# Optimization experiments

Measured on AMD Instinct MI355X. Metric: run time of the kernel, lower is better.

Reference implementation:

```python
import jax, jax.numpy as jnp
import numpy as np

N_HEAD = 16
SCALE = True
NEG = 10000.0


def setup_inputs() -> dict:
    key = jax.random.key(0)
    ks = jax.random.split(key, 5)
    B, S, D = 4, 1024, 1024
    x = jax.random.normal(ks[0], (B, S, D), dtype=jnp.float32)
    # GPT-2 Conv1D weights: W has shape [in, out], init ~N(0, 0.02)
    w_attn = jax.random.normal(ks[1], (D, 3 * D), dtype=jnp.float32) * 0.02
    b_attn = jnp.zeros((3 * D,), dtype=jnp.float32)
    w_proj = jax.random.normal(ks[2], (D, D), dtype=jnp.float32) * 0.02
    b_proj = jnp.zeros((D,), dtype=jnp.float32)
    return {"x": x, "w_attn": w_attn, "b_attn": b_attn,
            "w_proj": w_proj, "b_proj": b_proj}


def reference(x, w_attn, b_attn, w_proj, b_proj):
    B, S, D = x.shape
    H = N_HEAD
    hd = D // H
    # c_attn: Conv1D == x @ W + b
    qkv = jnp.einsum('bsd,de->bse', x, w_attn) + b_attn
    q, k, v = jnp.split(qkv, 3, axis=-1)
    # split heads -> [B, H, S, hd]
    q = q.reshape(B, S, H, hd).transpose(0, 2, 1, 3)
    k = k.reshape(B, S, H, hd).transpose(0, 2, 1, 3)
    v = v.reshape(B, S, H, hd).transpose(0, 2, 1, 3)
    # scores [B, H, S, S]
    w = jnp.einsum('bhqd,bhkd->bhqk', q, k)
    if SCALE:
        w = w / jnp.sqrt(jnp.float32(hd))
    # multiplicative causal mask: w*b - 10000*(1-b)
    bmask = jnp.tril(jnp.ones((S, S), dtype=w.dtype))[None, None]
    w = w * bmask - NEG * (1.0 - bmask)
    w = jax.nn.softmax(w, axis=-1)
    # attn_pdrop = 0 -> dropout is identity
    a = jnp.einsum('bhqk,bhkd->bhqd', w, v)
    # merge heads
    a = a.transpose(0, 2, 1, 3).reshape(B, S, D)
    # c_proj; resid_pdrop = 0
    out = jnp.einsum('bsd,de->bse', a, w_proj) + b_proj
    return out
```

## Files before the change

kernel.cpp:

```cpp
#include <hip/hip_runtime.h>
#include <hip/hip_bf16.h>


typedef __bf16 bf16x8 __attribute__((ext_vector_type(8)));
typedef float f32x4 __attribute__((ext_vector_type(4)));

__device__ __forceinline__ void load_lds16(const void* g, void* l) {
  __builtin_amdgcn_global_load_lds(
      (const __attribute__((address_space(1))) void*)g,
      (__attribute__((address_space(3))) void*)l, 16, 0, 0);
}

__global__ __launch_bounds__(256) void prep(
    const float* __restrict__ x, const float* __restrict__ w_attn,
    const float* __restrict__ w_proj, __bf16* __restrict__ Xb,
    __bf16* __restrict__ WT_attn, __bf16* __restrict__ WT_proj) {
  __shared__ __bf16 tile[32][33];
  const int blk = blockIdx.x;
  const int tid = threadIdx.x;
  if (blk < 4096) {
    const float* W;
    __bf16* WT;
    int n0, k0, N;
    if (blk < 3072) {
      W = w_attn; WT = WT_attn; N = 3072;
      n0 = (blk % 96) * 32; k0 = (blk / 96) * 32;
    } else {
      W = w_proj; WT = WT_proj; N = 1024;
      const int t = blk - 3072;
      n0 = (t & 31) * 32; k0 = (t >> 5) * 32;
    }
    const int tx = tid & 31, ty = tid >> 5;
#pragma unroll
    for (int j = 0; j < 32; j += 8)
      tile[ty + j][tx] = (__bf16)W[(size_t)(k0 + ty + j) * N + n0 + tx];
    __syncthreads();
#pragma unroll
    for (int j = 0; j < 32; j += 8)
      WT[(size_t)(n0 + ty + j) * 1024 + k0 + tx] = tile[tx][ty + j];
  } else {
    const size_t i = (size_t)(blk - 4096) * 4096 + tid * 16;
    const float4* xp = (const float4*)(x + i);
    float4 a = xp[0], b = xp[1], c = xp[2], d = xp[3];
    bf16x8 o0, o1;
    o0[0] = (__bf16)a.x; o0[1] = (__bf16)a.y; o0[2] = (__bf16)a.z; o0[3] = (__bf16)a.w;
    o0[4] = (__bf16)b.x; o0[5] = (__bf16)b.y; o0[6] = (__bf16)b.z; o0[7] = (__bf16)b.w;
    o1[0] = (__bf16)c.x; o1[1] = (__bf16)c.y; o1[2] = (__bf16)c.z; o1[3] = (__bf16)c.w;
    o1[4] = (__bf16)d.x; o1[5] = (__bf16)d.y; o1[6] = (__bf16)d.z; o1[7] = (__bf16)d.w;
    *(bf16x8*)(Xb + i) = o0;
    *(bf16x8*)(Xb + i + 8) = o1;
  }
}

__global__ __launch_bounds__(256) void transpose_v(
    const __bf16* __restrict__ Vr, __bf16* __restrict__ VT) {
  const int lane = threadIdx.x & 63, wave = threadIdx.x >> 6;
  const int bh = blockIdx.x >> 4;
  const int kb = (blockIdx.x & 15) * 64;
  const int b = bh >> 4, h = bh & 15;
  const __bf16* src =
      Vr + (size_t)(b * 1024 + kb + lane) * 1024 + h * 64 + wave * 16;
  bf16x8 v0 = *(const bf16x8*)src;
  bf16x8 v1 = *(const bf16x8*)(src + 8);
  __bf16* dst = VT + ((size_t)bh * 64 + wave * 16) * 1024 + kb + lane;
#pragma unroll
  for (int i = 0; i < 8; ++i) {
    dst[(size_t)i * 1024] = v0[i];
    dst[(size_t)(i + 8) * 1024] = v1[i];
  }
}

#define GEMM_CORE(A_, BT_, K_)                                                   \
  __shared__ __bf16 sA[128 * 32];                                               \
  __shared__ __bf16 sB[128 * 32];                                               \
  const int tid = threadIdx.x;                                                  \
  const int lane = tid & 63;                                                    \
  const int wave = tid >> 6;                                                    \
  const int waveM = wave >> 1, waveN = wave & 1;                                \
  const int quad = lane >> 4;                                                   \
  const int l16 = lane & 15;                                                    \
  const int rowBase = blockIdx.y * 128;                                         \
  const int colBase = blockIdx.x * 128;                                         \
  const int rIn = lane >> 2;                                                    \
  const int sIn = lane & 3;                                                     \
  const int gc = sIn ^ (rIn & 3) ^ ((rIn >> 2) & 3);                            \
  const int readSlot = quad ^ (l16 & 3) ^ ((l16 >> 2) & 3);                     \
  f32x4 acc[4][4] = {};                                                         \
  for (int k0 = 0; k0 < K_; k0 += 32) {                                         \
    __syncthreads();                                                            \
    _Pragma("unroll") for (int j = 0; j < 2; ++j) {                             \
      const int rb = wave * 32 + j * 16;                                        \
      load_lds16(&A_[(size_t)(rowBase + rb + rIn) * K_ + k0 + gc * 8],          \
                 &sA[rb * 32]);                                                 \
      load_lds16(&BT_[(size_t)(colBase + rb + rIn) * K_ + k0 + gc * 8],         \
                 &sB[rb * 32]);                                                 \
    }                                                                           \
    __syncthreads();                                                            \
    bf16x8 af[4], bfr[4];                                                       \
    _Pragma("unroll") for (int mt = 0; mt < 4; ++mt)                            \
      af[mt] = *(const bf16x8*)(&sA[(waveM * 64 + mt * 16 + l16) * 32 +         \
                                    readSlot * 8]);                             \
    _Pragma("unroll") for (int nt = 0; nt < 4; ++nt)                            \
      bfr[nt] = *(const bf16x8*)(&sB[(waveN * 64 + nt * 16 + l16) * 32 +        \
                                     readSlot * 8]);                            \
    _Pragma("unroll") for (int mt = 0; mt < 4; ++mt)                            \
    _Pragma("unroll") for (int nt = 0; nt < 4; ++nt)                            \
      acc[mt][nt] = __builtin_amdgcn_mfma_f32_16x16x32_bf16(                    \
          af[mt], bfr[nt], acc[mt][nt], 0, 0, 0);                               \
  }

__global__ __launch_bounds__(256) void gemm_qkv(
    const __bf16* __restrict__ A, const __bf16* __restrict__ BT,
    const float* __restrict__ bias, __bf16* __restrict__ Qp,
    __bf16* __restrict__ Kp, __bf16* __restrict__ Vr) {
  GEMM_CORE(A, BT, 1024)
  const int seg = colBase >> 10;
#pragma unroll
  for (int mt = 0; mt < 4; ++mt) {
    const int row0 = rowBase + waveM * 64 + mt * 16 + quad * 4;
#pragma unroll
    for (int nt = 0; nt < 4; ++nt) {
      const int col = colBase + waveN * 64 + nt * 16 + l16;
      const float bv = bias[col];
      const int cc = col & 1023;
#pragma unroll
      for (int r = 0; r < 4; ++r) {
        const int row = row0 + r;
        const float v = acc[mt][nt][r] + bv;
        if (seg == 2) {
          Vr[(size_t)row * 1024 + cc] = (__bf16)v;
        } else {
          const int bh = ((row >> 10) << 4) + (cc >> 6);
          __bf16* dst = (seg == 0) ? Qp : Kp;
          dst[((size_t)bh << 16) + (size_t)(row & 1023) * 64 + (cc & 63)] =
              (__bf16)v;
        }
      }
    }
  }
}

__global__ __launch_bounds__(256) void gemm_out(
    const __bf16* __restrict__ A, const __bf16* __restrict__ BT,
    const float* __restrict__ bias, float* __restrict__ C) {
  GEMM_CORE(A, BT, 1024)
#pragma unroll
  for (int mt = 0; mt < 4; ++mt) {
    const int row = rowBase + waveM * 64 + mt * 16 + quad * 4;
#pragma unroll
    for (int nt = 0; nt < 4; ++nt) {
      const int col = colBase + waveN * 64 + nt * 16 + l16;
      const float bv = bias[col];
#pragma unroll
      for (int r = 0; r < 4; ++r)
        C[(size_t)(row + r) * 1024 + col] = acc[mt][nt][r] + bv;
    }
  }
}

__global__ __launch_bounds__(256) void attn_mfma(
    const __bf16* __restrict__ Qp, const __bf16* __restrict__ Kp,
    const __bf16* __restrict__ VT, __bf16* __restrict__ Aout) {
  __shared__ __bf16 sK[128 * 64];
  __shared__ __bf16 sV[64 * 128];
  __shared__ __bf16 sP[4 * 16 * 128];

  const int tid = threadIdx.x;
  const int lane = tid & 63;
  const int wave = tid >> 6;
  const int quad = lane >> 4;
  const int l16 = lane & 15;
  const int swq = l16 & 7;

  const int bh = blockIdx.x >> 3;
  const int pr = blockIdx.x & 7;
  const int b = bh >> 4, h = bh & 15;
  const int qbA = pr * 64, qbB = (15 - pr) * 64;
  const int ktA_max = pr >> 1, ktB_max = (15 - pr) >> 1;

  const __bf16* Qb = Qp + ((size_t)bh << 16);
  const __bf16* Kb = Kp + ((size_t)bh << 16);
  const __bf16* VTb = VT + (size_t)bh * 64 * 1024;

  bf16x8 qA0A, qA1A, qA0B, qA1B;
  {
    const __bf16* qr = Qb + (size_t)(qbA + wave * 16 + l16) * 64 + quad * 8;
    qA0A = *(const bf16x8*)qr;
    qA1A = *(const bf16x8*)(qr + 32);
    qr = Qb + (size_t)(qbB + wave * 16 + l16) * 64 + quad * 8;
    qA0B = *(const bf16x8*)qr;
    qA1B = *(const bf16x8*)(qr + 32);
  }

  f32x4 OA[4] = {}, OB[4] = {};
  float psA[4] = {0.f, 0.f, 0.f, 0.f}, psB[4] = {0.f, 0.f, 0.f, 0.f};
  __bf16* pw = sP + wave * 2048;

  for (int kt = 0; kt <= ktB_max; ++kt) {
    const int kb = kt * 128;
    __syncthreads();

#pragma unroll
    for (int i = 0; i < 4; ++i) {
      const int rb = wave * 32 + i * 8;
      load_lds16(Kb + (size_t)(kb + rb + (lane >> 3)) * 64 +
                     (((lane & 7) ^ ((lane >> 3) & 7)) << 3),
                 &sK[rb * 64]);
    }
#pragma unroll
    for (int i = 0; i < 4; ++i) {
      const int db = wave * 16 + i * 4;
      const int d = db + (lane >> 4);
      load_lds16(VTb + (size_t)d * 1024 + kb + (((lane & 15) ^ (d & 7)) << 3),
                 &sV[db * 128]);
    }
    __syncthreads();

    {
      float sc[8][4];
#pragma unroll
      for (int n = 0; n < 8; ++n) {
        const int key = n * 16 + l16;
        bf16x8 kB0 = *(const bf16x8*)(&sK[key * 64 + ((quad ^ swq) << 3)]);
        bf16x8 kB1 = *(const bf16x8*)(&sK[key * 64 + (((quad + 4) ^ swq) << 3)]);
        f32x4 c = {};
        c = __builtin_amdgcn_mfma_f32_16x16x32_bf16(qA0B, kB0, c, 0, 0, 0);
        c = __builtin_amdgcn_mfma_f32_16x16x32_bf16(qA1B, kB1, c, 0, 0, 0);
#pragma unroll
        for (int r = 0; r < 4; ++r) sc[n][r] = c[r] * 0.125f;
      }
      if (kt == ktB_max) {
#pragma unroll
        for (int n = 0; n < 8; ++n) {
          const int kg = kb + n * 16 + l16;
#pragma unroll
          for (int r = 0; r < 4; ++r)
            if (kg > qbB + wave * 16 + quad * 4 + r) sc[n][r] = -1.0e30f;
        }
      }
#pragma unroll
      for (int n = 0; n < 8; ++n)
#pragma unroll
        for (int r = 0; r < 4; ++r) {
          float p = __expf(fminf(sc[n][r], 60.0f));
          sc[n][r] = p;
          psB[r] += p;
        }
      {
        const int kb8 = l16 >> 3, lo = l16 & 7;
#pragma unroll
        for (int n = 0; n < 8; ++n) {
          const int chunk = n * 2 + kb8;
#pragma unroll
          for (int r = 0; r < 4; ++r) {
            const int q = quad * 4 + r;
            pw[q * 128 + ((chunk ^ (q & 7)) << 3) + lo] = (__bf16)sc[n][r];
          }
        }
      }
#pragma unroll
      for (int cc = 0; cc < 4; ++cc) {
        bf16x8 pA = *(const bf16x8*)(&pw[l16 * 128 + (((cc * 4 + quad) ^ swq) << 3)]);
#pragma unroll
        for (int nt = 0; nt < 4; ++nt) {
          bf16x8 vB = *(const bf16x8*)(&sV[(nt * 16 + l16) * 128 +
                                           (((cc * 4 + quad) ^ swq) << 3)]);
          OB[nt] = __builtin_amdgcn_mfma_f32_16x16x32_bf16(pA, vB, OB[nt], 0, 0, 0);
        }
      }
    }

    if (kt <= ktA_max) {
      float sc[8][4];
#pragma unroll
      for (int n = 0; n < 8; ++n) {
        const int key = n * 16 + l16;
        bf16x8 kB0 = *(const bf16x8*)(&sK[key * 64 + ((quad ^ swq) << 3)]);
        bf16x8 kB1 = *(const bf16x8*)(&sK[key * 64 + (((quad + 4) ^ swq) << 3)]);
        f32x4 c = {};
        c = __builtin_amdgcn_mfma_f32_16x16x32_bf16(qA0A, kB0, c, 0, 0, 0);
        c = __builtin_amdgcn_mfma_f32_16x16x32_bf16(qA1A, kB1, c, 0, 0, 0);
#pragma unroll
        for (int r = 0; r < 4; ++r) sc[n][r] = c[r] * 0.125f;
      }
      if (kt == ktA_max) {
#pragma unroll
        for (int n = 0; n < 8; ++n) {
          const int kg = kb + n * 16 + l16;
#pragma unroll
          for (int r = 0; r < 4; ++r)
            if (kg > qbA + wave * 16 + quad * 4 + r) sc[n][r] = -1.0e30f;
        }
      }
#pragma unroll
      for (int n = 0; n < 8; ++n)
#pragma unroll
        for (int r = 0; r < 4; ++r) {
          float p = __expf(fminf(sc[n][r], 60.0f));
          sc[n][r] = p;
          psA[r] += p;
        }
      {
        const int kb8 = l16 >> 3, lo = l16 & 7;
#pragma unroll
        for (int n = 0; n < 8; ++n) {
          const int chunk = n * 2 + kb8;
#pragma unroll
          for (int r = 0; r < 4; ++r) {
            const int q = quad * 4 + r;
            pw[q * 128 + ((chunk ^ (q & 7)) << 3) + lo] = (__bf16)sc[n][r];
          }
        }
      }
#pragma unroll
      for (int cc = 0; cc < 4; ++cc) {
        bf16x8 pA = *(const bf16x8*)(&pw[l16 * 128 + (((cc * 4 + quad) ^ swq) << 3)]);
#pragma unroll
        for (int nt = 0; nt < 4; ++nt) {
          bf16x8 vB = *(const bf16x8*)(&sV[(nt * 16 + l16) * 128 +
                                           (((cc * 4 + quad) ^ swq) << 3)]);
          OA[nt] = __builtin_amdgcn_mfma_f32_16x16x32_bf16(pA, vB, OA[nt], 0, 0, 0);
        }
      }
    }
  }

  float invA[4], invB[4];
#pragma unroll
  for (int r = 0; r < 4; ++r) {
    float pa = psA[r], pb = psB[r];
    pa += __shfl_xor(pa, 1); pb += __shfl_xor(pb, 1);
    pa += __shfl_xor(pa, 2); pb += __shfl_xor(pb, 2);
    pa += __shfl_xor(pa, 4); pb += __shfl_xor(pb, 4);
    pa += __shfl_xor(pa, 8); pb += __shfl_xor(pb, 8);
    invA[r] = 1.0f / pa;
    invB[r] = 1.0f / pb;
  }
#pragma unroll
  for (int nt = 0; nt < 4; ++nt) {
#pragma unroll
    for (int r = 0; r < 4; ++r) {
      const int qA = qbA + wave * 16 + quad * 4 + r;
      const int qB = qbB + wave * 16 + quad * 4 + r;
      Aout[((size_t)b * 1024 + qA) * 1024 + h * 64 + nt * 16 + l16] =
          (__bf16)(OA[nt][r] * invA[r]);
      Aout[((size_t)b * 1024 + qB) * 1024 + h * 64 + nt * 16 + l16] =
          (__bf16)(OB[nt][r] * invB[r]);
    }
  }
}

extern "C" void kernel_launch(void* const* d_in, const int* in_sizes, int n_in,
                              void* d_out, int out_size, void* d_ws,
                              size_t ws_size, hipStream_t stream) {
  const float* x      = (const float*)d_in[0];
  const float* w_attn = (const float*)d_in[1];
  const float* b_attn = (const float*)d_in[2];
  const float* w_proj = (const float*)d_in[3];
  const float* b_proj = (const float*)d_in[4];
  float* out = (float*)d_out;

  char* ws = (char*)d_ws;
  __bf16* WT_attn = (__bf16*)(ws);
  __bf16* WT_proj = (__bf16*)(ws + 6291456);
  __bf16* Xb      = (__bf16*)(ws + 8388608);
  __bf16* Qp      = (__bf16*)(ws + 16777216);
  __bf16* Kp      = (__bf16*)(ws + 25165824);
  __bf16* Vr      = (__bf16*)(ws + 33554432);
  __bf16* Aattn   = (__bf16*)(ws + 41943040);
  __bf16* VT      = Xb;

  prep<<<5120, 256, 0, stream>>>(x, w_attn, w_proj, Xb, WT_attn, WT_proj);
  gemm_qkv<<<dim3(24, 32), 256, 0, stream>>>(Xb, WT_attn, b_attn, Qp, Kp, Vr);
  transpose_v<<<1024, 256, 0, stream>>>(Vr, VT);
  attn_mfma<<<512, 256, 0, stream>>>(Qp, Kp, VT, Aattn);
  gemm_out<<<dim3(8, 32), 256, 0, stream>>>(Aattn, WT_proj, b_proj, out);
}
```

Before: 180.3 us.

## Rewrite QKV GEMM as 256x256-tile 8-wave kernel with ping-pong LDS pipeline

Replaces the 128x128-tile QKV GEMM with a 512-thread kernel computing 256x256 tiles over 192 blocks. It double-buffers 64-wide K slices in 128 KB of LDS using direct global-to-LDS loads, XOR-swizzled LDS reads and a barrier-interleaved schedule that overlaps loads with MFMA quarter-phases. It also raises wave priority around MFMA bursts and remaps block indices for cache locality. The goal is to cut global traffic per FLOP and hide memory latency, at the cost of fewer blocks than CUs (192 tiles) and many barriers.

Result: no change. 178.9 us (-0.8%).

```diff
diff --git a/kernel.cpp b/kernel.cpp
--- a/kernel.cpp
+++ b/kernel.cpp
@@ -109,24 +109,156 @@
           af[mt], bfr[nt], acc[mt][nt], 0, 0, 0);                               \
   }
 
-__global__ __launch_bounds__(256) void gemm_qkv(
+
+#define BAR8 asm volatile("s_barrier" ::: "memory")
+#define LGKM0 asm volatile("s_waitcnt lgkmcnt(0)" ::: "memory")
+
+#define STG(GMAT, GROW0, K0, LOFF)                                             \
+  _Pragma("unroll") for (int i_ = 0; i_ < 2; ++i_)                             \
+    load_lds16((GMAT) + (size_t)((GROW0) + i_ * 64 + wave * 8 + srow) * 1024 + \
+                   (K0) + schunk * 8,                                          \
+               smem8 + (LOFF) + (i_ * 64 + wave * 8) * 64);
+
+#define LDA8(BASE, MH)                                                         \
+  _Pragma("unroll") for (int m_ = 0; m_ < 4; ++m_)                             \
+  _Pragma("unroll") for (int kk_ = 0; kk_ < 2; ++kk_)                          \
+    af[m_][kk_] = *(const bf16x8*)((BASE) + ((MH)*64 + m_ * 16 + l16) * 64 +   \
+                                   (((kk_ * 4 + quad) ^ rsw) * 8));
+
+#define LDB8(BASE, NLO)                                                        \
+  _Pragma("unroll") for (int n_ = 0; n_ < 2; ++n_)                             \
+  _Pragma("unroll") for (int kk_ = 0; kk_ < 2; ++kk_)                          \
+    bf[(NLO) + n_][kk_] =                                                      \
+        *(const bf16x8*)((BASE) + ((waveN & 1) * 64 + ((NLO) + n_) * 16 +      \
+                                   l16) * 64 +                                 \
+                         (((kk_ * 4 + quad) ^ rsw) * 8));
+
+#define MFMA_HALF(MH, NLO)                                                     \
+  __builtin_amdgcn_s_setprio(1);                                               \
+  _Pragma("unroll") for (int m_ = 0; m_ < 4; ++m_)                             \
+  _Pragma("unroll") for (int n_ = 0; n_ < 2; ++n_) {                           \
+    acc[(MH)*4 + m_][(NLO) + n_] = __builtin_amdgcn_mfma_f32_16x16x32_bf16(    \
+        af[m_][0], bf[(NLO) + n_][0], acc[(MH)*4 + m_][(NLO) + n_], 0, 0, 0);  \
+    acc[(MH)*4 + m_][(NLO) + n_] = __builtin_amdgcn_mfma_f32_16x16x32_bf16(    \
+        af[m_][1], bf[(NLO) + n_][1], acc[(MH)*4 + m_][(NLO) + n_], 0, 0, 0);  \
+  }                                                                            \
+  __builtin_amdgcn_s_setprio(0);
+
+__global__ __launch_bounds__(512, 2) void gemm_qkv8(
     const __bf16* __restrict__ A, const __bf16* __restrict__ BT,
     const float* __restrict__ bias, __bf16* __restrict__ Qp,
     __bf16* __restrict__ Kp, __bf16* __restrict__ Vr) {
-  GEMM_CORE(A, BT, 1024)
+  __shared__ __bf16 smem8[65536];
+  const int tid = threadIdx.x;
+  const int lane = tid & 63;
+  const int wave = tid >> 6;
+  const int waveM = wave >> 2;
+  const int waveN = wave & 3;
+  const int l16 = lane & 15;
+  const int quad = lane >> 4;
+  const int rsw = l16 & 7;
+  const int srow = lane >> 3;
+  const int schunk = (lane & 7) ^ srow;
+
+  const int bid = blockIdx.x;
+  const int swz = (bid & 7) * 24 + (bid >> 3);
+  const int tm = swz / 12, tn = swz - (swz / 12) * 12;
+  const int rowBase = tm * 256;
+  const int colBase = tn * 256;
+
+  const __bf16* aRd = smem8 + waveM * 8192;
+  const __bf16* bRd = smem8 + 16384 + (waveN >> 1) * 8192;
+
+  f32x4 acc[8][4] = {};
+  bf16x8 af[4][2], bf[4][2];
+
+  STG(A, rowBase, 0, 0);
+  STG(A, rowBase + 128, 0, 8192);
+  STG(BT, colBase, 0, 16384);
+  STG(BT, colBase + 128, 0, 24576);
+  STG(BT, colBase, 64, 32768 + 16384);
+  STG(BT, colBase + 128, 64, 32768 + 24576);
+  STG(A, rowBase, 64, 32768);
+  asm volatile("s_waitcnt vmcnt(6)" ::: "memory");
+  BAR8;
+
+  for (int t = 0; t < 8; ++t) {
+    const int kO = t * 128 + 64;
+    const int kS2 = t * 128 + 128;
+    const int kS3 = t * 128 + 192;
+    const bool s2 = kS2 < 1024;
+    const bool s3 = kS3 < 1024;
+
+    LDA8(aRd, 0);
+    LDB8(bRd, 0);
+    STG(A, rowBase + 128, kO, 32768 + 8192);
+    BAR8; LGKM0;
+    MFMA_HALF(0, 0);
+    BAR8;
+
+    LDB8(bRd, 2);
+    BAR8; LGKM0;
+    MFMA_HALF(0, 2);
+    BAR8;
+
+    LDA8(aRd, 1);
+    if (s2) { STG(BT, colBase, kS2, 16384); }
+    BAR8; LGKM0;
+    MFMA_HALF(1, 2);
+    BAR8;
+
+    if (s2) {
+      STG(BT, colBase + 128, kS2, 24576);
+      STG(A, rowBase, kS2, 0);
+      asm volatile("s_waitcnt vmcnt(6)" ::: "memory");
+    } else {
+      asm volatile("s_waitcnt vmcnt(0)" ::: "memory");
+    }
+    BAR8;
+    MFMA_HALF(1, 0);
+    BAR8;
+
+    LDA8(aRd + 32768, 0);
+    LDB8(bRd + 32768, 0);
+    if (s2) { STG(A, rowBase + 128, kS2, 8192); }
+    BAR8; LGKM0;
+    MFMA_HALF(0, 0);
+    BAR8;
+
+    LDB8(bRd + 32768, 2);
+    BAR8; LGKM0;
+    MFMA_HALF(0, 2);
+    BAR8;
+
+    LDA8(aRd + 32768, 1);
+    if (s3) { STG(BT, colBase, kS3, 32768 + 16384); }
+    BAR8; LGKM0;
+    MFMA_HALF(1, 2);
+    BAR8;
+
+    if (s3) {
+      STG(BT, colBase + 128, kS3, 32768 + 24576);
+      STG(A, rowBase, kS3, 32768);
+    }
+    asm volatile("s_waitcnt vmcnt(6)" ::: "memory");
+    BAR8;
+    MFMA_HALF(1, 0);
+    BAR8;
+  }
+
   const int seg = colBase >> 10;
 #pragma unroll
-  for (int mt = 0; mt < 4; ++mt) {
-    const int row0 = rowBase + waveM * 64 + mt * 16 + quad * 4;
-#pragma unroll
-    for (int nt = 0; nt < 4; ++nt) {
-      const int col = colBase + waveN * 64 + nt * 16 + l16;
+  for (int mm = 0; mm < 8; ++mm) {
+    const int row0 = rowBase + waveM * 128 + mm * 16 + quad * 4;
+#pragma unroll
+    for (int n = 0; n < 4; ++n) {
+      const int col = colBase + waveN * 64 + n * 16 + l16;
       const float bv = bias[col];
       const int cc = col & 1023;
 #pragma unroll
       for (int r = 0; r < 4; ++r) {
         const int row = row0 + r;
-        const float v = acc[mt][nt][r] + bv;
+        const float v = acc[mm][n][r] + bv;
         if (seg == 2) {
           Vr[(size_t)row * 1024 + cc] = (__bf16)v;
         } else {
@@ -371,7 +503,7 @@
   __bf16* VT      = Xb;
 
   prep<<<5120, 256, 0, stream>>>(x, w_attn, w_proj, Xb, WT_attn, WT_proj);
-  gemm_qkv<<<dim3(24, 32), 256, 0, stream>>>(Xb, WT_attn, b_attn, Qp, Kp, Vr);
+  gemm_qkv8<<<192, 512, 0, stream>>>(Xb, WT_attn, b_attn, Qp, Kp, Vr);
   transpose_v<<<1024, 256, 0, stream>>>(Vr, VT);
   attn_mfma<<<512, 256, 0, stream>>>(Qp, Kp, VT, Aattn);
   gemm_out<<<dim3(8, 32), 256, 0, stream>>>(Aattn, WT_proj, b_proj, out);
```
